# Kernel optimization log

Hardware: AMD Instinct MI355X
Metric: run time of the kernel (lower is better)

The kernel has to match this reference:

```python
import jax, jax.numpy as jnp
import numpy as np

# Module config (matches init_kwargs)
W_BIT = 2
PS_BIT = 8
IC = 256
OC = 256
K = 3
N_XBAR = 576
STRIDE = 1
PAD = 1
NUM_IC = min(IC, N_XBAR // (K * K))   # 64 input channels per crossbar array
GROUPS = IC // NUM_IC                 # 4 arrays (col_slide), ic divides evenly
QP_W = 2 ** W_BIT - 1                 # unsigned levels for nonneg pos/neg weights
QN_PS = -(2 ** (PS_BIT - 1))          # signed psum range
QP_PS = 2 ** (PS_BIT - 1) - 1


def lsq(v, s, qn, qp):
    """LSQ quantize-dequantize with straight-through rounding."""
    vs = jnp.clip(v / s, qn, qp)
    vbar = vs + jax.lax.stop_gradient(jnp.round(vs) - vs)
    return vbar * s


def conv2d(x, w):
    # x: [B, C, H, W], w: [O, C, k, k]
    return jax.lax.conv_general_dilated(
        x, w, window_strides=(STRIDE, STRIDE),
        padding=((PAD, PAD), (PAD, PAD)),
        dimension_numbers=('NCHW', 'OIHW', 'NCHW'))


def setup_inputs() -> dict:
    key = jax.random.key(0)
    k1, k2, k3, k4, k5 = jax.random.split(key, 5)
    x = jax.random.normal(k1, (16, IC, 56, 56), dtype=jnp.float32)
    weight = jax.random.normal(k2, (OC, IC, K, K), dtype=jnp.float32) * 0.05
    # positive LSQ step sizes, roughly 2*E|w|/sqrt(Qp) scale
    w_scale = jax.random.uniform(k3, (GROUPS,), dtype=jnp.float32) * 0.04 + 0.01
    ps_scale_p = jax.random.uniform(k4, (GROUPS,), dtype=jnp.float32) * 0.05 + 0.02
    ps_scale_n = jax.random.uniform(k5, (GROUPS,), dtype=jnp.float32) * 0.05 + 0.02
    return {"x": x, "weight": weight, "w_scale": w_scale,
            "ps_scale_p": ps_scale_p, "ps_scale_n": ps_scale_n}


def reference(x, weight, w_scale, ps_scale_p, ps_scale_n):
    B, _, H, W = x.shape
    # im2col tiling over input channels into GROUPS crossbar arrays
    xg = x.reshape(B, GROUPS, NUM_IC, H, W)                  # [B,G,cg,H,W]
    wg = weight.reshape(OC, GROUPS, NUM_IC, K, K)            # [O,G,cg,k,k]
    # pos / neg weight split, per-array LSQ weight quantization (shared quantizer)
    s_w = w_scale[:, None, None, None, None]                 # [G,1,1,1,1]
    wg_t = jnp.transpose(wg, (1, 0, 2, 3, 4))                # [G,O,cg,k,k]
    wq_p = lsq(jax.nn.relu(wg_t), s_w, 0, QP_W)
    wq_n = lsq(jax.nn.relu(-wg_t), s_w, 0, QP_W)
    xg_t = jnp.transpose(xg, (1, 0, 2, 3, 4))                # [G,B,cg,H,W]
    # per-array partial-sum convs (vmapped over arrays)
    vconv = jax.vmap(conv2d, in_axes=(0, 0))
    psum_p = vconv(xg_t, wq_p)                               # [G,B,O,h,w]
    psum_n = vconv(xg_t, wq_n)
    # per-array psum LSQ quantization ('Array' mode), then accumulate
    s_p = ps_scale_p[:, None, None, None, None]
    s_n = ps_scale_n[:, None, None, None, None]
    out_p = jnp.sum(lsq(psum_p, s_p, QN_PS, QP_PS), axis=0)  # [B,O,h,w]
    out_n = jnp.sum(lsq(psum_n, s_n, QN_PS, QP_PS), axis=0)
    return out_p - out_n
```

## Files before the change

### kernel.cpp

```cpp
#include <hip/hip_runtime.h>
#include <hip/hip_bf16.h>

typedef __attribute__((ext_vector_type(8))) short bf16x8_t;
typedef __attribute__((ext_vector_type(4))) float f32x4_t;
typedef __attribute__((ext_vector_type(4))) unsigned int u32x4_t;

#define XP_BYTES 55115776u
#define WT_BYTES 2359296u

typedef __attribute__((address_space(1))) const unsigned int ga_u32_t;
typedef __attribute__((address_space(3))) unsigned int lds_u32_t;

__device__ __forceinline__ void g2l16(const void* g, void* l) {
  __builtin_amdgcn_global_load_lds((ga_u32_t*)g, (lds_u32_t*)l, 16, 0, 0);
}

__global__ __launch_bounds__(256) void prep_x(const float* __restrict__ x,
                                              __hip_bfloat16* __restrict__ xp) {
  __shared__ float ls[64 * 57];
  int blk = blockIdx.x;
  int g = blk / 896;
  int r = blk - g * 896;
  int b = r / 56;
  int h = r - b * 56;
  int tid = threadIdx.x;
  const float* src = x + (size_t)(b * 256 + g * 64) * 3136 + h * 56;
  for (int i = tid; i < 64 * 56; i += 256) {
    int c = i / 56, w = i - c * 56;
    ls[c * 57 + w] = src[(size_t)c * 3136 + w];
  }
  __syncthreads();
  __hip_bfloat16* dst = xp + ((size_t)((g * 16 + b) * 58 + h + 1) * 58 + 1) * 128;
  int wp = tid >> 7;
  int inner = tid & 127;
  int hl = inner >> 6, c = inner & 63;
  for (int w0 = 0; w0 < 56; w0 += 2) {
    int w = w0 + wp;
    float v = ls[c * 57 + w];
    __hip_bfloat16 hi = __float2bfloat16(v);
    __hip_bfloat16 val = hl ? __float2bfloat16(v - __bfloat162float(hi)) : hi;
    dst[(size_t)w * 128 + inner] = val;
  }
}

__global__ __launch_bounds__(256) void prep_w(const float* __restrict__ wgt,
                                              const float* __restrict__ wsc,
                                              unsigned short* __restrict__ wtf) {
  int idx = blockIdx.x * 256 + threadIdx.x;
  if (idx >= 147456) return;
  int l = idx & 63;
  int ni = (idx >> 6) & 3;
  int wq = (idx >> 8) & 3;
  int u = idx >> 10;
  int g = u / 36;
  int r36 = u - g * 36;
  int sgn = (r36 >= 18) ? 1 : 0;
  int r18 = r36 - sgn * 18;
  int tap = r18 >> 1, cc = r18 & 1;
  int oc = wq * 64 + ni * 16 + (l & 15);
  float inv = 1.f / wsc[g];
  unsigned short pk[8];
#pragma unroll
  for (int e = 0; e < 8; ++e) {
    int c = cc * 32 + ((l >> 4) << 3) + e;
    float w = wgt[(size_t)oc * 2304 + (g * 64 + c) * 9 + tap] * inv;
    if (sgn) w = -w;
    float q = rintf(fminf(fmaxf(w, 0.f), 3.f));
    union { __hip_bfloat16 h; unsigned short s; } cv;
    cv.h = __float2bfloat16(q);
    pk[e] = cv.s;
  }
  u32x4_t v;
  v[0] = (unsigned)pk[0] | ((unsigned)pk[1] << 16);
  v[1] = (unsigned)pk[2] | ((unsigned)pk[3] << 16);
  v[2] = (unsigned)pk[4] | ((unsigned)pk[5] << 16);
  v[3] = (unsigned)pk[6] | ((unsigned)pk[7] << 16);
  *(u32x4_t*)(wtf + (size_t)idx * 8) = v;
}

#define MEMPIN asm volatile("" ::: "memory")
#define BAR __builtin_amdgcn_s_barrier()
#define VMCNT4 asm volatile("s_waitcnt vmcnt(4)" ::: "memory")
#define VMCNT0 asm volatile("s_waitcnt vmcnt(0)" ::: "memory")

__global__ __launch_bounds__(256, 2) void conv_mfma(
    const unsigned short* __restrict__ xp, const unsigned short* __restrict__ wtf,
    const float* __restrict__ wsc, const float* __restrict__ psp,
    const float* __restrict__ psn, float* __restrict__ out) {
  __shared__ char Astrip[65536];

  const int bid = blockIdx.x;
  const int wg = (bid & 7) * 98 + (bid >> 3);
  const int b = wg / 49;
  const int t = wg - b * 49;
  const int r0 = (t << 6) / 56;

  const int tid = threadIdx.x;
  const int wv = tid >> 6;
  const int l = tid & 63;

  int pxb[4];
#pragma unroll
  for (int mi = 0; mi < 4; ++mi) {
    int m = (t << 6) + mi * 16 + (l & 15);
    int rv = m / 56, w = m - rv * 56;
    pxb[mi] = ((rv - r0) << 6) + w;
  }

  float w0s = wsc[0], w1s = wsc[1], w2s = wsc[2], w3s = wsc[3];
  float p0 = psp[0], p1 = psp[1], p2 = psp[2], p3 = psp[3];
  float n0 = psn[0], n1 = psn[1], n2 = psn[2], n3 = psn[3];

  f32x4_t acc[4][4], oacc[4][4];
  const f32x4_t fz = {0.f, 0.f, 0.f, 0.f};
#pragma unroll
  for (int i = 0; i < 4; ++i)
#pragma unroll
    for (int j = 0; j < 4; ++j) { acc[i][j] = fz; oacc[i][j] = fz; }

  const char* xg = (const char*)xp;
  const char* wtb = (const char*)wtf + (wv << 12) + (l << 4);
  const unsigned a_gbbase = (unsigned)((b * 3364 + r0 * 58) * 256);

#define STAGE_STRIP(gg)                                                        \
  {                                                                            \
    const char* s_ = xg + (unsigned)(gg)*13778944u + a_gbbase;                 \
    _Pragma("unroll")                                                          \
    for (int k_ = 0; k_ < 16; ++k_) {                                          \
      int idx_ = tid + (k_ << 8);                                              \
      int px_ = idx_ >> 4, sl_ = idx_ & 15;                                    \
      int sr_ = px_ >> 6, xc_ = px_ & 63;                                      \
      g2l16(s_ + (sr_ * 58 + xc_) * 256 +                                      \
                (((sl_ & 8) | ((sl_ & 7) ^ (xc_ & 7))) << 4),                  \
            Astrip + idx_ * 16);                                               \
    }                                                                          \
  }

#define LOADB(d0, d1, d2, d3, uu)                                              \
  {                                                                            \
    const char* p_ = wtb + (unsigned)(uu) * 16384u;                            \
    d0 = *(const bf16x8_t*)(p_);                                               \
    d1 = *(const bf16x8_t*)(p_ + 1024);                                        \
    d2 = *(const bf16x8_t*)(p_ + 2048);                                        \
    d3 = *(const bf16x8_t*)(p_ + 3072);                                        \
  }

#define READA(cc_, tyo_)                                                       \
  {                                                                            \
    const int kj_ = ((cc_) << 2) + (l >> 4);                                   \
    _Pragma("unroll")                                                          \
    for (int mi = 0; mi < 4; ++mi) {                                           \
      int px_ = pxb[mi] + (tyo_);                                              \
      int base_ = (px_ << 8) + ((kj_ ^ (px_ & 7)) << 4);                       \
      ahi[mi] = *(const bf16x8_t*)(Astrip + base_);                            \
      alo[mi] = *(const bf16x8_t*)(Astrip + base_ + 128);                      \
    }                                                                          \
  }

#define MMA32(B0, B1, B2, B3)                                                  \
  __builtin_amdgcn_s_setprio(1);                                               \
  _Pragma("unroll")                                                            \
  for (int mi = 0; mi < 4; ++mi) {                                             \
    acc[mi][0] = __builtin_amdgcn_mfma_f32_16x16x32_bf16(ahi[mi], B0, acc[mi][0], 0, 0, 0); \
    acc[mi][1] = __builtin_amdgcn_mfma_f32_16x16x32_bf16(ahi[mi], B1, acc[mi][1], 0, 0, 0); \
    acc[mi][2] = __builtin_amdgcn_mfma_f32_16x16x32_bf16(ahi[mi], B2, acc[mi][2], 0, 0, 0); \
    acc[mi][3] = __builtin_amdgcn_mfma_f32_16x16x32_bf16(ahi[mi], B3, acc[mi][3], 0, 0, 0); \
    acc[mi][0] = __builtin_amdgcn_mfma_f32_16x16x32_bf16(alo[mi], B0, acc[mi][0], 0, 0, 0); \
    acc[mi][1] = __builtin_amdgcn_mfma_f32_16x16x32_bf16(alo[mi], B1, acc[mi][1], 0, 0, 0); \
    acc[mi][2] = __builtin_amdgcn_mfma_f32_16x16x32_bf16(alo[mi], B2, acc[mi][2], 0, 0, 0); \
    acc[mi][3] = __builtin_amdgcn_mfma_f32_16x16x32_bf16(alo[mi], B3, acc[mi][3], 0, 0, 0); \
  }                                                                            \
  __builtin_amdgcn_s_setprio(0);

#define QUANTIZE(gg, ss)                                                       \
  {                                                                            \
    float sw = ((gg) & 2) ? (((gg) & 1) ? w3s : w2s) : (((gg) & 1) ? w1s : w0s); \
    float sp = ((gg) & 2) ? (((gg) & 1) ? p3 : p2) : (((gg) & 1) ? p1 : p0);   \
    float sn = ((gg) & 2) ? (((gg) & 1) ? n3 : n2) : (((gg) & 1) ? n1 : n0);   \
    float sq = (ss) ? sn : sp;                                                 \
    float rs = sw / sq;                                                        \
    float sm = (ss) ? -sq : sq;                                                \
    _Pragma("unroll")                                                          \
    for (int mi = 0; mi < 4; ++mi)                                             \
      _Pragma("unroll")                                                        \
      for (int ni = 0; ni < 4; ++ni)                                           \
        _Pragma("unroll")                                                      \
        for (int j = 0; j < 4; ++j) {                                          \
          float v = acc[mi][ni][j] * rs;                                       \
          v = fminf(fmaxf(v, -128.f), 127.f);                                  \
          oacc[mi][ni][j] += sm * rintf(v);                                    \
          acc[mi][ni][j] = 0.f;                                                \
        }                                                                      \
  }

  bf16x8_t ahi[4], alo[4];
  bf16x8_t bA0, bA1, bA2, bA3, bB0, bB1, bB2, bB3;

  STAGE_STRIP(0);
  MEMPIN;
  LOADB(bA0, bA1, bA2, bA3, 0);
  LOADB(bB0, bB1, bB2, bB3, 1);

  int tap = 0, sgn = 0, g = 0;
  for (int v = 0; v < 72; ++v) {
    const int ty = tap / 3;
    const int tyo = (ty << 6) + (tap - ty * 3);

    VMCNT4;
    if (tap == 0) { BAR; }
    MEMPIN;
    READA(0, tyo);
    MMA32(bA0, bA1, bA2, bA3);
    MEMPIN;
    if (v < 71) { LOADB(bA0, bA1, bA2, bA3, 2 * v + 2); }

    if (v == 71) { VMCNT0; } else { VMCNT4; }
    MEMPIN;
    READA(1, tyo);
    MMA32(bB0, bB1, bB2, bB3);

    if (tap == 8) {
      QUANTIZE(g, sgn);
      if (sgn == 1 && v < 71) {
        BAR;
        STAGE_STRIP(g + 1);
      }
    }
    MEMPIN;
    if (v < 71) { LOADB(bB0, bB1, bB2, bB3, 2 * v + 3); }

    if (++tap == 9) { tap = 0; g += sgn; sgn ^= 1; }
  }

#pragma unroll
  for (int ni = 0; ni < 4; ++ni) {
    int oc = (wv << 6) + ni * 16 + (l & 15);
    float* orow = out + ((size_t)(b * 256 + oc)) * 3136;
#pragma unroll
    for (int mi = 0; mi < 4; ++mi) {
      int m0 = (t << 6) + mi * 16 + ((l >> 4) << 2);
#pragma unroll
      for (int j = 0; j < 4; ++j) {
        orow[m0 + j] = oacc[mi][ni][j];
      }
    }
  }
#undef STAGE_STRIP
#undef LOADB
#undef READA
#undef MMA32
#undef QUANTIZE
}

__global__ __launch_bounds__(256) void naive_conv(
    const float* __restrict__ x, const float* __restrict__ wgt,
    const float* __restrict__ wsc, const float* __restrict__ psp,
    const float* __restrict__ psn, float* __restrict__ out) {
  int idx = blockIdx.x * 256 + threadIdx.x;
  if (idx >= 12845056) return;
  int b = idx / 802816;
  int r = idx - b * 802816;
  int oc = r / 3136;
  int hw = r - oc * 3136;
  int h = hw / 56, w = hw - (hw / 56) * 56;
  float o = 0.f;
  for (int g = 0; g < 4; ++g) {
    float sw = wsc[g];
    float inv = 1.f / sw;
    float pp = 0.f, pn = 0.f;
    for (int tap = 0; tap < 9; ++tap) {
      int y = h + tap / 3 - 1, xx = w + tap % 3 - 1;
      if (y < 0 || y > 55 || xx < 0 || xx > 55) continue;
      const float* xr = x + (size_t)(b * 256 + g * 64) * 3136 + y * 56 + xx;
      const float* wrr = wgt + (size_t)oc * 2304 + (size_t)(g * 64) * 9 + tap;
      for (int c = 0; c < 64; ++c) {
        float xv = xr[(size_t)c * 3136];
        float rv = wrr[c * 9] * inv;
        pp += xv * rintf(fminf(fmaxf(rv, 0.f), 3.f));
        pn += xv * rintf(fminf(fmaxf(-rv, 0.f), 3.f));
      }
    }
    float sp = psp[g], sn = psn[g];
    o += rintf(fminf(fmaxf(pp * (sw / sp), -128.f), 127.f)) * sp;
    o -= rintf(fminf(fmaxf(pn * (sw / sn), -128.f), 127.f)) * sn;
  }
  out[idx] = o;
}

extern "C" void kernel_launch(void* const* d_in, const int* in_sizes, int n_in,
                              void* d_out, int out_size, void* d_ws, size_t ws_size,
                              hipStream_t stream) {
  const float* x = (const float*)d_in[0];
  const float* wgt = (const float*)d_in[1];
  const float* wsc = (const float*)d_in[2];
  const float* psp = (const float*)d_in[3];
  const float* psn = (const float*)d_in[4];
  float* out = (float*)d_out;

  if (ws_size >= (size_t)XP_BYTES + (size_t)WT_BYTES) {
    unsigned short* xpw = (unsigned short*)d_ws;
    unsigned short* wtw = (unsigned short*)((char*)d_ws + XP_BYTES);
    hipMemsetAsync(d_ws, 0, XP_BYTES, stream);
    prep_x<<<3584, 256, 0, stream>>>(x, (__hip_bfloat16*)xpw);
    prep_w<<<576, 256, 0, stream>>>(wgt, wsc, wtw);
    conv_mfma<<<784, 256, 0, stream>>>(xpw, wtw, wsc, psp, psn, out);
  } else {
    naive_conv<<<(12845056 + 255) / 256, 256, 0, stream>>>(x, wgt, wsc, psp, psn, out);
  }
}
```

Baseline: 249.5 us.

## Switch conv MFMA to 32x32x16 tiles and zero padding in prep_x

The main conv kernel now uses 32x32x16 bf16 MFMA instead of 16x16x32. The weight pre-pack layout and the LDS A-fragment reads are re-tiled to match, and the output is written as vectorized float4 stores. The separate full-workspace hipMemsetAsync is removed, and prep_x now writes the zero halo rows and columns itself. This aims to cut per-FLOP instruction and LDS-read overhead and drop a 55MB memset, at the risk of register pressure from 16-wide accumulators and layout bugs.

```diff
diff --git a/kernel.cpp b/kernel.cpp
--- a/kernel.cpp
+++ b/kernel.cpp
@@ -3,6 +3,7 @@
 
 typedef __attribute__((ext_vector_type(8))) short bf16x8_t;
 typedef __attribute__((ext_vector_type(4))) float f32x4_t;
+typedef __attribute__((ext_vector_type(16))) float f32x16_t;
 typedef __attribute__((ext_vector_type(4))) unsigned int u32x4_t;
 
 #define XP_BYTES 55115776u
@@ -30,7 +31,8 @@
     ls[c * 57 + w] = src[(size_t)c * 3136 + w];
   }
   __syncthreads();
-  __hip_bfloat16* dst = xp + ((size_t)((g * 16 + b) * 58 + h + 1) * 58 + 1) * 128;
+  __hip_bfloat16* gbbase = xp + (size_t)(g * 16 + b) * 58 * 58 * 128;
+  __hip_bfloat16* dst = gbbase + ((size_t)(h + 1) * 58 + 1) * 128;
   int wp = tid >> 7;
   int inner = tid & 127;
   int hl = inner >> 6, c = inner & 63;
@@ -41,6 +43,19 @@
     __hip_bfloat16 val = hl ? __float2bfloat16(v - __bfloat162float(hi)) : hi;
     dst[(size_t)w * 128 + inner] = val;
   }
+  __hip_bfloat16 z = __float2bfloat16(0.0f);
+  {
+    __hip_bfloat16* rowp = gbbase + (size_t)(h + 1) * 58 * 128;
+    if (tid < 128) rowp[inner] = z;
+    else           rowp[57 * 128 + inner] = z;
+  }
+  if (h == 0) {
+    for (int i = tid; i < 58 * 128; i += 256) gbbase[i] = z;
+  }
+  if (h == 55) {
+    __hip_bfloat16* r57 = gbbase + (size_t)57 * 58 * 128;
+    for (int i = tid; i < 58 * 128; i += 256) r57[i] = z;
+  }
 }
 
 __global__ __launch_bounds__(256) void prep_w(const float* __restrict__ wgt,
@@ -49,7 +64,7 @@
   int idx = blockIdx.x * 256 + threadIdx.x;
   if (idx >= 147456) return;
   int l = idx & 63;
-  int ni = (idx >> 6) & 3;
+  int part = (idx >> 6) & 3;
   int wq = (idx >> 8) & 3;
   int u = idx >> 10;
   int g = u / 36;
@@ -57,12 +72,13 @@
   int sgn = (r36 >= 18) ? 1 : 0;
   int r18 = r36 - sgn * 18;
   int tap = r18 >> 1, cc = r18 & 1;
-  int oc = wq * 64 + ni * 16 + (l & 15);
+  int nj = part >> 1, kseg = part & 1;
+  int oc = wq * 64 + nj * 32 + (l & 31);
   float inv = 1.f / wsc[g];
   unsigned short pk[8];
 #pragma unroll
   for (int e = 0; e < 8; ++e) {
-    int c = cc * 32 + ((l >> 4) << 3) + e;
+    int c = cc * 32 + kseg * 16 + ((l >> 5) << 3) + e;
     float w = wgt[(size_t)oc * 2304 + (g * 64 + c) * 9 + tap] * inv;
     if (sgn) w = -w;
     float q = rintf(fminf(fmaxf(w, 0.f), 3.f));
@@ -99,10 +115,10 @@
   const int wv = tid >> 6;
   const int l = tid & 63;
 
-  int pxb[4];
-#pragma unroll
-  for (int mi = 0; mi < 4; ++mi) {
-    int m = (t << 6) + mi * 16 + (l & 15);
+  int pxb[2];
+#pragma unroll
+  for (int mi = 0; mi < 2; ++mi) {
+    int m = (t << 6) + mi * 32 + (l & 31);
     int rv = m / 56, w = m - rv * 56;
     pxb[mi] = ((rv - r0) << 6) + w;
   }
@@ -111,12 +127,13 @@
   float p0 = psp[0], p1 = psp[1], p2 = psp[2], p3 = psp[3];
   float n0 = psn[0], n1 = psn[1], n2 = psn[2], n3 = psn[3];
 
-  f32x4_t acc[4][4], oacc[4][4];
-  const f32x4_t fz = {0.f, 0.f, 0.f, 0.f};
-#pragma unroll
-  for (int i = 0; i < 4; ++i)
-#pragma unroll
-    for (int j = 0; j < 4; ++j) { acc[i][j] = fz; oacc[i][j] = fz; }
+  f32x16_t acc[2][2], oacc[2][2];
+#pragma unroll
+  for (int i = 0; i < 2; ++i)
+#pragma unroll
+    for (int j = 0; j < 2; ++j)
+#pragma unroll
+      for (int e = 0; e < 16; ++e) { acc[i][j][e] = 0.f; oacc[i][j][e] = 0.f; }
 
   const char* xg = (const char*)xp;
   const char* wtb = (const char*)wtf + (wv << 12) + (l << 4);
@@ -139,36 +156,39 @@
 #define LOADB(d0, d1, d2, d3, uu)                                              \
   {                                                                            \
     const char* p_ = wtb + (unsigned)(uu) * 16384u;                            \
-    d0 = *(const bf16x8_t*)(p_);                                               \
-    d1 = *(const bf16x8_t*)(p_ + 1024);                                        \
-    d2 = *(const bf16x8_t*)(p_ + 2048);                                        \
-    d3 = *(const bf16x8_t*)(p_ + 3072);                                        \
+    d0 = *(const bf16x8_t*)(p_);                                \
+    d1 = *(const bf16x8_t*)(p_ + 1024);                         \
+    d2 = *(const bf16x8_t*)(p_ + 2048);                         \
+    d3 = *(const bf16x8_t*)(p_ + 3072);                         \
   }
 
 #define READA(cc_, tyo_)                                                       \
   {                                                                            \
-    const int kj_ = ((cc_) << 2) + (l >> 4);                                   \
     _Pragma("unroll")                                                          \
-    for (int mi = 0; mi < 4; ++mi) {                                           \
+    for (int mi = 0; mi < 2; ++mi) {                                           \
       int px_ = pxb[mi] + (tyo_);                                              \
-      int base_ = (px_ << 8) + ((kj_ ^ (px_ & 7)) << 4);                       \
-      ahi[mi] = *(const bf16x8_t*)(Astrip + base_);                            \
-      alo[mi] = *(const bf16x8_t*)(Astrip + base_ + 128);                      \
+      _Pragma("unroll")                                                        \
+      for (int ks = 0; ks < 2; ++ks) {                                         \
+        int slot_ = (((cc_) << 2) + (ks << 1) + (l >> 5)) ^ (px_ & 7);         \
+        int base_ = (px_ << 8) + (slot_ << 4);                                 \
+        ahi[mi][ks] = *(const bf16x8_t*)(Astrip + base_);                      \
+        alo[mi][ks] = *(const bf16x8_t*)(Astrip + base_ + 128);                \
+      }                                                                        \
     }                                                                          \
   }
 
-#define MMA32(B0, B1, B2, B3)                                                  \
+#define MMA16(B0, B1, B2, B3)                                                  \
   __builtin_amdgcn_s_setprio(1);                                               \
   _Pragma("unroll")                                                            \
-  for (int mi = 0; mi < 4; ++mi) {                                             \
-    acc[mi][0] = __builtin_amdgcn_mfma_f32_16x16x32_bf16(ahi[mi], B0, acc[mi][0], 0, 0, 0); \
-    acc[mi][1] = __builtin_amdgcn_mfma_f32_16x16x32_bf16(ahi[mi], B1, acc[mi][1], 0, 0, 0); \
-    acc[mi][2] = __builtin_amdgcn_mfma_f32_16x16x32_bf16(ahi[mi], B2, acc[mi][2], 0, 0, 0); \
-    acc[mi][3] = __builtin_amdgcn_mfma_f32_16x16x32_bf16(ahi[mi], B3, acc[mi][3], 0, 0, 0); \
-    acc[mi][0] = __builtin_amdgcn_mfma_f32_16x16x32_bf16(alo[mi], B0, acc[mi][0], 0, 0, 0); \
-    acc[mi][1] = __builtin_amdgcn_mfma_f32_16x16x32_bf16(alo[mi], B1, acc[mi][1], 0, 0, 0); \
-    acc[mi][2] = __builtin_amdgcn_mfma_f32_16x16x32_bf16(alo[mi], B2, acc[mi][2], 0, 0, 0); \
-    acc[mi][3] = __builtin_amdgcn_mfma_f32_16x16x32_bf16(alo[mi], B3, acc[mi][3], 0, 0, 0); \
+  for (int mi = 0; mi < 2; ++mi) {                                             \
+    acc[mi][0] = __builtin_amdgcn_mfma_f32_32x32x16_bf16(ahi[mi][0], B0, acc[mi][0], 0, 0, 0); \
+    acc[mi][1] = __builtin_amdgcn_mfma_f32_32x32x16_bf16(ahi[mi][0], B2, acc[mi][1], 0, 0, 0); \
+    acc[mi][0] = __builtin_amdgcn_mfma_f32_32x32x16_bf16(ahi[mi][1], B1, acc[mi][0], 0, 0, 0); \
+    acc[mi][1] = __builtin_amdgcn_mfma_f32_32x32x16_bf16(ahi[mi][1], B3, acc[mi][1], 0, 0, 0); \
+    acc[mi][0] = __builtin_amdgcn_mfma_f32_32x32x16_bf16(alo[mi][0], B0, acc[mi][0], 0, 0, 0); \
+    acc[mi][1] = __builtin_amdgcn_mfma_f32_32x32x16_bf16(alo[mi][0], B2, acc[mi][1], 0, 0, 0); \
+    acc[mi][0] = __builtin_amdgcn_mfma_f32_32x32x16_bf16(alo[mi][1], B1, acc[mi][0], 0, 0, 0); \
+    acc[mi][1] = __builtin_amdgcn_mfma_f32_32x32x16_bf16(alo[mi][1], B3, acc[mi][1], 0, 0, 0); \
   }                                                                            \
   __builtin_amdgcn_s_setprio(0);
 
@@ -181,19 +201,19 @@
     float rs = sw / sq;                                                        \
     float sm = (ss) ? -sq : sq;                                                \
     _Pragma("unroll")                                                          \
-    for (int mi = 0; mi < 4; ++mi)                                             \
+    for (int mi = 0; mi < 2; ++mi)                                             \
       _Pragma("unroll")                                                        \
-      for (int ni = 0; ni < 4; ++ni)                                           \
+      for (int nj = 0; nj < 2; ++nj)                                           \
         _Pragma("unroll")                                                      \
-        for (int j = 0; j < 4; ++j) {                                          \
-          float v = acc[mi][ni][j] * rs;                                       \
+        for (int e = 0; e < 16; ++e) {                                         \
+          float v = acc[mi][nj][e] * rs;                                       \
           v = fminf(fmaxf(v, -128.f), 127.f);                                  \
-          oacc[mi][ni][j] += sm * rintf(v);                                    \
-          acc[mi][ni][j] = 0.f;                                                \
+          oacc[mi][nj][e] += sm * rintf(v);                                    \
+          acc[mi][nj][e] = 0.f;                                                \
         }                                                                      \
   }
 
-  bf16x8_t ahi[4], alo[4];
+  bf16x8_t ahi[2][2], alo[2][2];
   bf16x8_t bA0, bA1, bA2, bA3, bB0, bB1, bB2, bB3;
 
   STAGE_STRIP(0);
@@ -210,14 +230,14 @@
     if (tap == 0) { BAR; }
     MEMPIN;
     READA(0, tyo);
-    MMA32(bA0, bA1, bA2, bA3);
+    MMA16(bA0, bA1, bA2, bA3);
     MEMPIN;
     if (v < 71) { LOADB(bA0, bA1, bA2, bA3, 2 * v + 2); }
 
     if (v == 71) { VMCNT0; } else { VMCNT4; }
     MEMPIN;
     READA(1, tyo);
-    MMA32(bB0, bB1, bB2, bB3);
+    MMA16(bB0, bB1, bB2, bB3);
 
     if (tap == 8) {
       QUANTIZE(g, sgn);
@@ -233,22 +253,27 @@
   }
 
 #pragma unroll
-  for (int ni = 0; ni < 4; ++ni) {
-    int oc = (wv << 6) + ni * 16 + (l & 15);
+  for (int nj = 0; nj < 2; ++nj) {
+    int oc = (wv << 6) + nj * 32 + (l & 31);
     float* orow = out + ((size_t)(b * 256 + oc)) * 3136;
 #pragma unroll
-    for (int mi = 0; mi < 4; ++mi) {
-      int m0 = (t << 6) + mi * 16 + ((l >> 4) << 2);
-#pragma unroll
-      for (int j = 0; j < 4; ++j) {
-        orow[m0 + j] = oacc[mi][ni][j];
+    for (int mi = 0; mi < 2; ++mi) {
+#pragma unroll
+      for (int q = 0; q < 4; ++q) {
+        int m0 = (t << 6) + mi * 32 + q * 8 + ((l >> 5) << 2);
+        f32x4_t vst;
+        vst[0] = oacc[mi][nj][q * 4 + 0];
+        vst[1] = oacc[mi][nj][q * 4 + 1];
+        vst[2] = oacc[mi][nj][q * 4 + 2];
+        vst[3] = oacc[mi][nj][q * 4 + 3];
+        *(f32x4_t*)(orow + m0) = vst;
       }
     }
   }
 #undef STAGE_STRIP
 #undef LOADB
 #undef READA
-#undef MMA32
+#undef MMA16
 #undef QUANTIZE
 }
 
@@ -300,7 +325,6 @@
   if (ws_size >= (size_t)XP_BYTES + (size_t)WT_BYTES) {
     unsigned short* xpw = (unsigned short*)d_ws;
     unsigned short* wtw = (unsigned short*)((char*)d_ws + XP_BYTES);
-    hipMemsetAsync(d_ws, 0, XP_BYTES, stream);
     prep_x<<<3584, 256, 0, stream>>>(x, (__hip_bfloat16*)xpw);
     prep_w<<<576, 256, 0, stream>>>(wgt, wsc, wtw);
     conv_mfma<<<784, 256, 0, stream>>>(xpw, wtw, wsc, psp, psn, out);
```

Result: slower. 263.5 us (+5.6%).
